# Performance work log

Measured on AMD Instinct MI355X. Metric: run time of the kernel, lower is better.

Reference implementation:

```python
import jax, jax.numpy as jnp
import numpy as np

# --- static config (matches init_kwargs) ---
C = 384        # channels
H = 8          # num_heads
HD = C // H    # head_dim = 48
K = 1024       # patch_size (window)
BASE = 100.0   # rope_freq
MAX_POS = 4096
GRID_SIZE = 0.02
LN_EPS = 1e-5


def _interleave8(x, y, z):
    """Morton-interleave the low 8 bits of x,y,z -> 24-bit code (int32)."""
    key = jnp.zeros_like(x)
    for i in range(8):
        m = 1 << i
        key = key | ((x & m) << (2 * i + 2)) | ((y & m) << (2 * i + 1)) | ((z & m) << (2 * i))
    return key


def _serialize_points(xyz):
    """xyz: (B,3,N) -> (order (B,N) int32, grid (B,N,3) int32). Z-order sort."""
    pts = jnp.transpose(xyz, (0, 2, 1))                       # (B,N,3)
    grid = ((pts - pts.min(axis=1, keepdims=True)) / GRID_SIZE).astype(jnp.int32)
    grid = jnp.clip(grid, 0, 65535)
    gx, gy, gz = grid[..., 0], grid[..., 1], grid[..., 2]
    lo = _interleave8(gx & 255, gy & 255, gz & 255)           # low 24 bits of Morton code
    hi = _interleave8((gx >> 8) & 255, (gy >> 8) & 255, (gz >> 8) & 255)  # high word
    # 48-bit Morton order == lexsort with hi as primary key, lo secondary
    order = jax.vmap(lambda l, h: jnp.lexsort((l, h)))(lo, hi)
    return order.astype(jnp.int32), grid


def _rope_tables(d):
    inv_freq = 1.0 / (BASE ** (jnp.arange(0, d, 2, dtype=jnp.float32) / d))
    t = jnp.arange(MAX_POS, dtype=jnp.float32)
    freqs = t[:, None] * inv_freq[None, :]                    # (MAX_POS, d/2)
    freqs = jnp.concatenate([freqs, freqs], axis=-1)          # (MAX_POS, d)
    return jnp.cos(freqs), jnp.sin(freqs)


def _rotate_half(x):
    h = x.shape[-1] // 2
    return jnp.concatenate([-x[..., h:], x[..., :h]], axis=-1)


def _point_rope(tok, pos):
    """tok: (B,H,N,D) with D%3==0; pos: (B,N,3) int grid coords."""
    D = tok.shape[-1]
    d = D // 3
    pos = jnp.clip(pos, 0, MAX_POS - 1)
    cos, sin = _rope_tables(d)
    outs = []
    for axis, ch in enumerate(jnp.split(tok, 3, axis=-1)):
        p = pos[:, :, axis]                                   # (B,N)
        c = cos[p][:, None]                                   # (B,1,N,d)
        s = sin[p][:, None]
        outs.append(ch * c + _rotate_half(ch) * s)
    return jnp.concatenate(outs, axis=-1)


def _layernorm(x, g, b):
    mu = x.mean(axis=-1, keepdims=True)
    var = ((x - mu) ** 2).mean(axis=-1, keepdims=True)
    return (x - mu) * jax.lax.rsqrt(var + LN_EPS) * g + b


def _forward(x, xyz, ln1_g, ln1_b, qkv_w, qkv_b, proj_w, proj_b,
             ln2_g, ln2_b, ffn_w1, ffn_b1, ffn_w2, ffn_b2):
    B, C_, N = x.shape
    order, grid = _serialize_points(xyz)
    x_sorted = jnp.take_along_axis(x, order[:, None, :], axis=2)          # (B,C,N)
    grid_sorted = jnp.take_along_axis(grid, order[:, :, None], axis=1)    # (B,N,3)
    x_t = jnp.transpose(x_sorted, (0, 2, 1))                              # (B,N,C)
    shortcut = x_t
    xn = _layernorm(x_t, ln1_g, ln1_b)
    pad = (K - N % K) % K
    if pad > 0:
        xn = jnp.pad(xn, ((0, 0), (0, pad), (0, 0)))
        grid_sorted = jnp.pad(grid_sorted, ((0, 0), (0, pad), (0, 0)))
    Np = xn.shape[1]
    nw = Np // K
    qkv = (xn @ qkv_w + qkv_b).reshape(B, Np, 3, H, HD)
    q = jnp.transpose(qkv[:, :, 0], (0, 2, 1, 3))                         # (B,H,Np,HD)
    k = jnp.transpose(qkv[:, :, 1], (0, 2, 1, 3))
    v = jnp.transpose(qkv[:, :, 2], (0, 2, 1, 3))
    q = _point_rope(q, grid_sorted)
    k = _point_rope(k, grid_sorted)
    qw = q.reshape(B, H, nw, K, HD)
    kw = k.reshape(B, H, nw, K, HD)
    vw = v.reshape(B, H, nw, K, HD)
    scale = 1.0 / np.sqrt(HD).astype(np.float32)
    scores = jnp.einsum('bhwqd,bhwkd->bhwqk', qw, kw) * scale             # (B,H,nw,K,K)
    attn = jax.nn.softmax(scores, axis=-1)
    out = jnp.einsum('bhwqk,bhwkd->bhwqd', attn, vw)                      # (B,H,nw,K,HD)
    out = jnp.transpose(out, (0, 2, 3, 1, 4)).reshape(B, Np, C)
    out = out[:, :N]
    out = out @ proj_w + proj_b
    x_t = shortcut + out
    x_t = x_t + (jax.nn.gelu(_layernorm(x_t, ln2_g, ln2_b) @ ffn_w1 + ffn_b1,
                             approximate=False) @ ffn_w2 + ffn_b2)
    x_out = jnp.transpose(x_t, (0, 2, 1))                                 # (B,C,N)
    inv_order = jnp.argsort(order, axis=1)
    x_out = jnp.take_along_axis(x_out, inv_order[:, None, :], axis=2)
    return x_out


def setup_inputs() -> dict:
    key = jax.random.key(0)
    ks = jax.random.split(key, 12)
    B, N = 1, 16384
    s = 0.02
    return {
        'x': jax.random.normal(ks[0], (B, C, N), dtype=jnp.float32),
        'xyz': jax.random.uniform(ks[1], (B, 3, N), dtype=jnp.float32),
        'ln1_g': jnp.ones((C,), jnp.float32),
        'ln1_b': jnp.zeros((C,), jnp.float32),
        'qkv_w': jax.random.normal(ks[2], (C, 3 * C), jnp.float32) * s,
        'qkv_b': jnp.zeros((3 * C,), jnp.float32),
        'proj_w': jax.random.normal(ks[3], (C, C), jnp.float32) * s,
        'proj_b': jnp.zeros((C,), jnp.float32),
        'ln2_g': jnp.ones((C,), jnp.float32),
        'ln2_b': jnp.zeros((C,), jnp.float32),
        'ffn_w1': jax.random.normal(ks[4], (C, 4 * C), jnp.float32) * s,
        'ffn_b1': jnp.zeros((4 * C,), jnp.float32),
        'ffn_w2': jax.random.normal(ks[5], (4 * C, C), jnp.float32) * s,
        'ffn_b2': jnp.zeros((C,), jnp.float32),
    }


def reference(x, xyz, ln1_g, ln1_b, qkv_w, qkv_b, proj_w, proj_b,
              ln2_g, ln2_b, ffn_w1, ffn_b1, ffn_w2, ffn_b2):
    return _forward(x, xyz, ln1_g, ln1_b, qkv_w, qkv_b, proj_w, proj_b,
                    ln2_g, ln2_b, ffn_w1, ffn_b1, ffn_w2, ffn_b2)
```

## Files before the change

### kernel.cpp

```cpp
#include <hip/hip_runtime.h>
#include <hip/hip_bf16.h>

typedef unsigned short u16;
typedef unsigned int u32;
typedef unsigned long long u64;
typedef __attribute__((ext_vector_type(8))) short s16x8;
typedef __attribute__((ext_vector_type(4))) short s16x4;
typedef __attribute__((ext_vector_type(8))) unsigned short u16x8;
typedef __attribute__((ext_vector_type(4))) unsigned short u16x4;
typedef __attribute__((ext_vector_type(4))) float fx4;
typedef __attribute__((ext_vector_type(4))) unsigned int ux4;
typedef __attribute__((ext_vector_type(2))) unsigned int ux2;

__device__ __forceinline__ float bf2f(u16 u){ u32 x=((u32)u)<<16; return __builtin_bit_cast(float,x); }
__device__ __forceinline__ u16 f2bf(float f){ u32 x=__builtin_bit_cast(u32,f); return (u16)((x + 0x7FFFu + ((x>>16)&1u))>>16); }
__device__ __forceinline__ u32 cvtpk(float lo, float hi){
  u32 r; asm("v_cvt_pk_bf16_f32 %0, %1, %2" : "=v"(r) : "v"(lo), "v"(hi)); return r;
}

__device__ __forceinline__ s16x8 ld_bf8(const u16* p){
  s16x4 lo = *(const s16x4*)p;
  s16x4 hi = *(const s16x4*)(p+4);
  s16x8 r;
  r[0]=lo[0]; r[1]=lo[1]; r[2]=lo[2]; r[3]=lo[3];
  r[4]=hi[0]; r[5]=hi[1]; r[6]=hi[2]; r[7]=hi[3];
  return r;
}

__device__ __forceinline__ void gload16(const void* g, void* l){
  __builtin_amdgcn_global_load_lds((__attribute__((address_space(1))) void*)g,
                                   (__attribute__((address_space(3))) void*)l, 16, 0, 0);
}

__device__ __forceinline__ u64 spread3(u32 v){
  u64 x = v & 0xFFFFull;
  x = (x | (x<<32)) & 0x001f00000000ffffull;
  x = (x | (x<<16)) & 0x001f0000ff0000ffull;
  x = (x | (x<<8))  & 0x100f00f00f00f00full;
  x = (x | (x<<4))  & 0x10c30c30c30c30c3ull;
  x = (x | (x<<2))  & 0x1249249249249249ull;
  return x;
}

__global__ __launch_bounds__(256) void min3_kernel(const float* __restrict__ xyz, u32* __restrict__ mins, int N)
{
  int i = blockIdx.x*256 + threadIdx.x;
  float v0 = xyz[i], v1 = xyz[N+i], v2 = xyz[2*N+i];
  #pragma unroll
  for (int s=1;s<64;s<<=1){
    v0 = fminf(v0, __shfl_xor(v0,s));
    v1 = fminf(v1, __shfl_xor(v1,s));
    v2 = fminf(v2, __shfl_xor(v2,s));
  }
  if ((threadIdx.x & 63) == 0){
    atomicMin(mins+0, __builtin_bit_cast(u32, v0));
    atomicMin(mins+1, __builtin_bit_cast(u32, v1));
    atomicMin(mins+2, __builtin_bit_cast(u32, v2));
  }
}

__global__ __launch_bounds__(256) void keys_grid_kernel(const float* __restrict__ xyz, const u32* __restrict__ mins,
        u64* __restrict__ keys, int* __restrict__ gridO, int N)
{
  int i = blockIdx.x*256 + threadIdx.x;
  float mx0 = __builtin_bit_cast(float, mins[0]);
  float mx1 = __builtin_bit_cast(float, mins[1]);
  float mx2 = __builtin_bit_cast(float, mins[2]);
  int gx=(int)((xyz[i]-mx0)/0.02f);     gx = gx<0?0:(gx>65535?65535:gx);
  int gy=(int)((xyz[N+i]-mx1)/0.02f);   gy = gy<0?0:(gy>65535?65535:gy);
  int gz=(int)((xyz[2*N+i]-mx2)/0.02f); gz = gz<0?0:(gz>65535?65535:gz);
  gridO[i*3+0]=gx; gridO[i*3+1]=gy; gridO[i*3+2]=gz;
  u64 mort = (spread3((u32)gx)<<2)|(spread3((u32)gy)<<1)|spread3((u32)gz);
  keys[i] = (mort<<14) | (u64)i;
}

__global__ __launch_bounds__(1024) void bsort_kernel(u64* __restrict__ keys)
{
  __shared__ u64 sk[2048];
  int t = threadIdx.x;
  u64* base = keys + (size_t)blockIdx.x*2048;
  sk[t] = base[t]; sk[t+1024] = base[t+1024];
  for (int size=2; size<=2048; size<<=1){
    for (int stride=size>>1; stride>0; stride>>=1){
      __syncthreads();
      int i = 2*t - (t & (stride-1));
      int j = i + stride;
      u64 a = sk[i], b = sk[j];
      bool up = ((i & size) == 0);
      if ((a > b) == up){ sk[i]=b; sk[j]=a; }
    }
  }
  __syncthreads();
  base[t] = sk[t]; base[t+1024] = sk[t+1024];
}

template<bool FINAL>
__global__ __launch_bounds__(256) void merge_kernel(const u64* __restrict__ src, u64* __restrict__ dst,
        int* __restrict__ order, int L, int N)
{
  int gt = blockIdx.x*256 + threadIdx.x;
  int d0 = gt*8;
  if (d0 >= N) return;
  int pair = d0 / (2*L);
  int base = pair*2*L;
  int ld = d0 - base;
  const u64* A = src + base;
  const u64* B = A + L;
  int lo = ld > L ? ld - L : 0;
  int hi = ld < L ? ld : L;
  while (lo < hi){
    int mid = (lo+hi)>>1;
    if (A[mid] <= B[ld-1-mid]) lo = mid+1; else hi = mid;
  }
  int i = lo, j = ld - lo;
  u64* out = dst + base + ld;
  int* oout = order + base + ld;
  u64 a = (i < L) ? A[i] : ~0ull;
  u64 b = (j < L) ? B[j] : ~0ull;
  #pragma unroll
  for (int e=0;e<8;e++){
    u64 v;
    if (a <= b){ v = a; i++; a = (i<L)?A[i]:~0ull; }
    else       { v = b; j++; b = (j<L)?B[j]:~0ull; }
    out[e] = v;
    if (FINAL) oout[e] = (int)(v & 16383ull);
  }
}

__global__ __launch_bounds__(256) void wtrans4_kernel(const float* __restrict__ qkv_w, const float* __restrict__ proj_w,
    const float* __restrict__ w1, const float* __restrict__ w2,
    u16* __restrict__ qkv_wT, u16* __restrict__ proj_wT, u16* __restrict__ w1T, u16* __restrict__ w2T)
{
  __shared__ float tl[32][33];
  int bid = blockIdx.x;
  const float* W; u16* Wt; int K, Nc, lb;
  if (bid < 432)      { W=qkv_w;  Wt=qkv_wT;  K=384;  Nc=1152; lb=bid; }
  else if (bid < 576) { W=proj_w; Wt=proj_wT; K=384;  Nc=384;  lb=bid-432; }
  else if (bid < 1152){ W=w1;     Wt=w1T;     K=384;  Nc=1536; lb=bid-576; }
  else                { W=w2;     Wt=w2T;     K=1536; Nc=384;  lb=bid-1152; }
  int nb = Nc/32;
  int n0 = (lb % nb)*32;
  int k0 = (lb / nb)*32;
  int t=threadIdx.x; int r=t>>5, c=t&31;
  #pragma unroll
  for (int p=0;p<4;p++) tl[p*8+r][c] = W[(size_t)(k0+p*8+r)*Nc + n0+c];
  __syncthreads();
  #pragma unroll
  for (int p=0;p<4;p++) Wt[(size_t)(n0+p*8+r)*K + k0+c] = f2bf(tl[c][p*8+r]);
}

template<bool BF16IN>
__global__ __launch_bounds__(256) void ln32_kernel(const void* __restrict__ xin, const float* __restrict__ g,
     const float* __restrict__ b, u16* __restrict__ xn, int N)
{
  extern __shared__ char dsm[];
  float* tile = (float*)dsm;
  int n0 = blockIdx.x*32;
  int t = threadIdx.x;
  int tok32 = t&31, cg2 = t>>5;
  #pragma unroll 8
  for (int p=0;p<48;p++){
    int cc = p*8 + cg2;
    float v;
    if (BF16IN) v = bf2f(((const u16*)xin)[(size_t)cc*N + n0 + tok32]);
    else        v = ((const float*)xin)[(size_t)cc*N + n0 + tok32];
    tile[tok32*388 + cc] = v;
  }
  __syncthreads();
  int tok = t>>3, part = t&7;
  const float* row = tile + tok*388 + part*48;
  float s=0.f;
  #pragma unroll
  for (int j=0;j<48;j++) s += row[j];
  s += __shfl_xor(s,1); s += __shfl_xor(s,2); s += __shfl_xor(s,4);
  float mu = s*(1.0f/384.0f);
  float vr=0.f;
  #pragma unroll
  for (int j=0;j<48;j++){ float d=row[j]-mu; vr += d*d; }
  vr += __shfl_xor(vr,1); vr += __shfl_xor(vr,2); vr += __shfl_xor(vr,4);
  float rs = rsqrtf(vr*(1.0f/384.0f) + 1e-5f);
  u16* dst = xn + (size_t)(n0+tok)*384 + part*48;
  #pragma unroll
  for (int q=0;q<6;q++){
    float v[8];
    #pragma unroll
    for (int j=0;j<8;j++){
      int c = part*48 + q*8 + j;
      v[j] = (row[q*8+j]-mu)*rs*g[c] + b[c];
    }
    ux4 o;
    o[0]=cvtpk(v[0],v[1]); o[1]=cvtpk(v[2],v[3]); o[2]=cvtpk(v[4],v[5]); o[3]=cvtpk(v[6],v[7]);
    *(ux4*)(dst + q*8) = o;
  }
}

__device__ __forceinline__ float gelu_f(float v){
  return 0.5f*v*(1.0f + erff(v*0.7071067811865475f));
}

template<int EPI>
__global__ __launch_bounds__(256) void gemm128_kernel(const u16* __restrict__ A, const u16* __restrict__ Bt,
    const float* __restrict__ bias, u16* __restrict__ outB, float* __restrict__ outF,
    const float* __restrict__ resF, const u16* __restrict__ resB, int M, int Nout, int K)
{
  __shared__ u16 Al[128*64];
  __shared__ u16 Bl[128*64];
  int nmt = M>>7;
  int m0 = (blockIdx.x % nmt)<<7;
  int n0 = (blockIdx.x / nmt)<<7;
  int t = threadIdx.x, lane=t&63, wv=t>>6, wr=wv>>1, wc=wv&1;
  int fr = lane&15, fg = lane>>4;
  fx4 acc[4][4];
  #pragma unroll
  for (int i=0;i<4;i++)
  #pragma unroll
  for (int j=0;j<4;j++) acc[i][j]=(fx4){0.f,0.f,0.f,0.f};
  int srow = wv*32 + (lane>>3);
  int swz  = ((lane&7) ^ ((lane>>3)&7)) * 8;
  const u16* ApL = A  + (size_t)(m0+srow)*K + swz;
  const u16* BpL = Bt + (size_t)(n0+srow)*K + swz;
  u16* AlW = Al + wv*2048 + lane*8;
  u16* BlW = Bl + wv*2048 + lane*8;
  const u16* a_base = Al + (wr*64+fr)*64;
  const u16* b_base = Bl + (wc*64+fr)*64;
  int swr = fr & 7;
  for (int k0=0;k0<K;k0+=64){
    #pragma unroll
    for (int i=0;i<4;i++){
      gload16(ApL + k0 + (size_t)i*8*K, AlW + i*512);
      gload16(BpL + k0 + (size_t)i*8*K, BlW + i*512);
    }
    __syncthreads();
    #pragma unroll
    for (int ks=0;ks<2;ks++){
      int soff = (((ks*4+fg) ^ swr) << 3);
      s16x8 a[4], b[4];
      #pragma unroll
      for (int mi=0;mi<4;mi++) a[mi] = *(const s16x8*)(a_base + mi*1024 + soff);
      #pragma unroll
      for (int ni=0;ni<4;ni++) b[ni] = *(const s16x8*)(b_base + ni*1024 + soff);
      #pragma unroll
      for (int mi=0;mi<4;mi++)
      #pragma unroll
      for (int ni=0;ni<4;ni++)
        acc[mi][ni] = __builtin_amdgcn_mfma_f32_16x16x32_bf16(a[mi], b[ni], acc[mi][ni], 0,0,0);
    }
    __syncthreads();
  }
  if (EPI==0 || EPI==1){
    #pragma unroll
    for (int mi=0;mi<4;mi++)
    #pragma unroll
    for (int ni=0;ni<4;ni++){
      int c = n0 + wc*64 + ni*16 + fr;
      float bi = bias[c];
      int mb = m0 + wr*64 + mi*16 + fg*4;
      #pragma unroll
      for (int j=0;j<4;j++){
        float vv = acc[mi][ni][j] + bi;
        if (EPI==1) vv = gelu_f(vv);
        outB[(size_t)(mb+j)*Nout + c] = f2bf(vv);
      }
    }
  } else if (EPI==2){
    #pragma unroll
    for (int mi=0;mi<4;mi++)
    #pragma unroll
    for (int ni=0;ni<4;ni++){
      int c = n0 + wc*64 + ni*16 + fr;
      float bi = bias[c];
      size_t idx = (size_t)c*M + m0 + wr*64 + mi*16 + fg*4;
      fx4 r4 = *(const fx4*)(resF + idx);
      ux2 p;
      p[0] = cvtpk(acc[mi][ni][0]+bi+r4[0], acc[mi][ni][1]+bi+r4[1]);
      p[1] = cvtpk(acc[mi][ni][2]+bi+r4[2], acc[mi][ni][3]+bi+r4[3]);
      *(ux2*)(outB + idx) = p;
    }
  } else {
    #pragma unroll
    for (int mi=0;mi<4;mi++)
    #pragma unroll
    for (int ni=0;ni<4;ni++){
      int c = n0 + wc*64 + ni*16 + fr;
      float bi = bias[c];
      size_t idx = (size_t)c*M + m0 + wr*64 + mi*16 + fg*4;
      ux2 rb = *(const ux2*)(resB + idx);
      fx4 o;
      o[0] = acc[mi][ni][0] + bi + bf2f((u16)rb[0]);
      o[1] = acc[mi][ni][1] + bi + bf2f((u16)(rb[0]>>16));
      o[2] = acc[mi][ni][2] + bi + bf2f((u16)rb[1]);
      o[3] = acc[mi][ni][3] + bi + bf2f((u16)(rb[1]>>16));
      *(fx4*)(outF + idx) = o;
    }
  }
}

#define LOG2_100_O8 0.8304820237218405f

__global__ __launch_bounds__(256) void rope_kernel(const u16* __restrict__ qkv, const int* __restrict__ order,
    const int* __restrict__ gridO, u16* __restrict__ Qp, u16* __restrict__ Kp, u16* __restrict__ Vp, int N)
{
  __shared__ float csm[64][24][2];
  __shared__ int origs[64];
  int i0 = blockIdx.x<<6;
  int t = threadIdx.x;
  if (t<64) origs[t] = order[i0+t];
  __syncthreads();
  for (int idx=t; idx<64*24; idx+=256){
    int tok = idx/24, slot = idx - tok*24;
    int a = slot>>3, fi = slot&7;
    int pos = gridO[(size_t)origs[tok]*3 + a];
    pos = pos<0?0:(pos>4095?4095:pos);
    float invf = __builtin_amdgcn_exp2f(-(float)fi * LOG2_100_O8);
    float ang = (float)pos * invf;
    csm[tok][slot][0] = __cosf(ang);
    csm[tok][slot][1] = __sinf(ang);
  }
  __syncthreads();
  int tok = t&63;
  int i = i0 + tok;
  const u16* src = qkv + (size_t)origs[tok]*1152;
  for (int h=t>>6; h<8; h+=4){
    size_t dst = ((size_t)h*N + i)*48;
    #pragma unroll
    for (int a=0;a<3;a++){
      u16x8 qa = *(const u16x8*)(src + h*48 + a*16);
      u16x8 qb = *(const u16x8*)(src + h*48 + a*16 + 8);
      u16x8 ka = *(const u16x8*)(src + 384 + h*48 + a*16);
      u16x8 kb = *(const u16x8*)(src + 384 + h*48 + a*16 + 8);
      float oqa[8], oqb[8], oka[8], okb[8];
      #pragma unroll
      for (int j=0;j<8;j++){
        float c0 = csm[tok][a*8+j][0], s0 = csm[tok][a*8+j][1];
        float ql = bf2f(qa[j]), qh = bf2f(qb[j]);
        float kl = bf2f(ka[j]), kh = bf2f(kb[j]);
        oqa[j] = ql*c0 - qh*s0;
        oqb[j] = qh*c0 + ql*s0;
        oka[j] = kl*c0 - kh*s0;
        okb[j] = kh*c0 + kl*s0;
      }
      ux4 OQa, OQb, OKa, OKb;
      #pragma unroll
      for (int p=0;p<4;p++){
        OQa[p]=cvtpk(oqa[2*p],oqa[2*p+1]);
        OQb[p]=cvtpk(oqb[2*p],oqb[2*p+1]);
        OKa[p]=cvtpk(oka[2*p],oka[2*p+1]);
        OKb[p]=cvtpk(okb[2*p],okb[2*p+1]);
      }
      *(ux4*)(Qp + dst + a*16) = OQa;
      *(ux4*)(Qp + dst + a*16 + 8) = OQb;
      *(ux4*)(Kp + dst + a*16) = OKa;
      *(ux4*)(Kp + dst + a*16 + 8) = OKb;
      u16x8 va = *(const u16x8*)(src + 768 + h*48 + a*16);
      u16x8 vb = *(const u16x8*)(src + 768 + h*48 + a*16 + 8);
      *(u16x8*)(Vp + dst + a*16) = va;
      *(u16x8*)(Vp + dst + a*16 + 8) = vb;
    }
  }
}

#define ATTN_SCALE 0.14433756729740643f
#define E2SCALE 0.2082354550504211f
#define DEFER_RAW 55.0f
#define KSTRIDE 68

__global__ __launch_bounds__(512) void attn7_kernel(const u16* __restrict__ Qp, const u16* __restrict__ Kp,
    const u16* __restrict__ Vp, const int* __restrict__ order, u16* __restrict__ attn, int N, int nw)
{
  __shared__ u16 Kl[2][64*KSTRIDE];
  __shared__ u16 Vl[2][48*KSTRIDE];
  __shared__ u16 Pl[8][32*KSTRIDE];
  int b = blockIdx.x;
  int hw = b & 127;
  int qc = b >> 7;
  int w = hw % nw, h = hw / nw;
  int t = threadIdx.x, lane = t&63, wv = t>>6;
  int fr = lane & 15, fg = lane >> 4;
  size_t base = ((size_t)h*N + (size_t)w*1024);
  int q0 = qc*256 + wv*32;
  bool kact = t < 384;
  int krow = t/6, kc = t - krow*6;
  const u16* ksrc = Kp + (base + krow)*48 + kc*8;
  int koff = krow*KSTRIDE + kc*8;
  int s2 = t - 128;
  bool vact = t >= 128;
  int vrow = s2/6, vc = s2 - vrow*6;
  const u16* vsrc = Vp + (base + vrow)*48 + vc*8;
  int vkey = vrow ^ (vc<<3);
  if (t < 256){
    ux2 z = {0,0};
    *(ux2*)&Kl[0][(t>>2)*KSTRIDE + 48 + (t&3)*4] = z;
    *(ux2*)&Kl[1][(t>>2)*KSTRIDE + 48 + (t&3)*4] = z;
  }
  s16x8 qf[2][2];
  s16x8 zf = {0,0,0,0,0,0,0,0};
  #pragma unroll
  for (int n=0;n<2;n++){
    const u16* qrow = Qp + (base + q0 + n*16 + fr)*48;
    qf[n][0] = ld_bf8(qrow + fg*8);
    qf[n][1] = (fg < 2) ? ld_bf8(qrow + 32 + fg*8) : zf;
  }
  s16x8 ones;
  #pragma unroll
  for (int j=0;j<8;j++) ones[j] = (short)0x3F80;

  float m0r = -3.4e38f, m1r = -3.4e38f;
  fx4 o00=(fx4){0.f,0.f,0.f,0.f}, o01=o00, o02=o00, o03=o00, o10=o00, o11=o00, o12=o00, o13=o00;
  u16* pl = Pl[wv];
  ux4 kreg = {0,0,0,0}, vreg = {0,0,0,0};
  if (kact) kreg = *(const ux4*)ksrc;
  if (vact) vreg = *(const ux4*)vsrc;
  if (kact){
    ux2 lo; lo[0]=kreg[0]; lo[1]=kreg[1];
    ux2 hi; hi[0]=kreg[2]; hi[1]=kreg[3];
    *(ux2*)(Kl[0]+koff) = lo; *(ux2*)(Kl[0]+koff+4) = hi;
  }
  if (vact){
    u16* vcp = Vl[0] + vkey;
    vcp[(vc*8+0)*KSTRIDE] = (u16)vreg[0];
    vcp[(vc*8+1)*KSTRIDE] = (u16)(vreg[0]>>16);
    vcp[(vc*8+2)*KSTRIDE] = (u16)vreg[1];
    vcp[(vc*8+3)*KSTRIDE] = (u16)(vreg[1]>>16);
    vcp[(vc*8+4)*KSTRIDE] = (u16)vreg[2];
    vcp[(vc*8+5)*KSTRIDE] = (u16)(vreg[2]>>16);
    vcp[(vc*8+6)*KSTRIDE] = (u16)vreg[3];
    vcp[(vc*8+7)*KSTRIDE] = (u16)(vreg[3]>>16);
  }
  __syncthreads();

  for (int c=0;c<16;c++){
    int cur = c & 1;
    const u16* kl = Kl[cur];
    const u16* vl = Vl[cur];
    if (c < 15){
      if (kact) kreg = *(const ux4*)(ksrc + (size_t)(c+1)*3072);
      if (vact) vreg = *(const ux4*)(vsrc + (size_t)(c+1)*3072);
    }
    fx4 s0[4], s1v[4];
    __builtin_amdgcn_s_setprio(1);
    #pragma unroll
    for (int m=0;m<4;m++){
      s0[m]=(fx4){0.f,0.f,0.f,0.f}; s1v[m]=s0[m];
      #pragma unroll
      for (int s=0;s<2;s++){
        s16x8 af = ld_bf8(kl + (m*16+fr)*KSTRIDE + s*32 + fg*8);
        s0[m]  = __builtin_amdgcn_mfma_f32_16x16x32_bf16(af, qf[0][s], s0[m],  0,0,0);
        s1v[m] = __builtin_amdgcn_mfma_f32_16x16x32_bf16(af, qf[1][s], s1v[m], 0,0,0);
      }
    }
    __builtin_amdgcn_s_setprio(0);
    float pm0 = -3.4e38f, pm1 = -3.4e38f;
    #pragma unroll
    for (int m=0;m<4;m++){
      float a0 = fmaxf(fmaxf(s0[m][0],s0[m][1]), fmaxf(s0[m][2],s0[m][3]));
      float a1 = fmaxf(fmaxf(s1v[m][0],s1v[m][1]), fmaxf(s1v[m][2],s1v[m][3]));
      pm0 = fmaxf(pm0, a0); pm1 = fmaxf(pm1, a1);
    }
    pm0 = fmaxf(pm0, __shfl_xor(pm0,16)); pm0 = fmaxf(pm0, __shfl_xor(pm0,32));
    pm1 = fmaxf(pm1, __shfl_xor(pm1,16)); pm1 = fmaxf(pm1, __shfl_xor(pm1,32));
    if (!__all((pm0 <= m0r + DEFER_RAW) & (pm1 <= m1r + DEFER_RAW))){
      float nm0 = fmaxf(m0r, pm0), nm1 = fmaxf(m1r, pm1);
      float f0 = __builtin_amdgcn_exp2f((m0r - nm0)*E2SCALE);
      float f1 = __builtin_amdgcn_exp2f((m1r - nm1)*E2SCALE);
      m0r = nm0; m1r = nm1;
      #pragma unroll
      for (int j=0;j<4;j++){
        float g0 = __shfl(f0, fg*4+j);
        float g1 = __shfl(f1, fg*4+j);
        o00[j]*=g0; o01[j]*=g0; o02[j]*=g0; o03[j]*=g0;
        o10[j]*=g1; o11[j]*=g1; o12[j]*=g1; o13[j]*=g1;
      }
    }
    #pragma unroll
    for (int m=0;m<4;m++){
      float e0[4], e1[4];
      #pragma unroll
      for (int j=0;j<4;j++){
        e0[j] = __builtin_amdgcn_exp2f((s0[m][j]-m0r)*E2SCALE);
        e1[j] = __builtin_amdgcn_exp2f((s1v[m][j]-m1r)*E2SCALE);
      }
      ux2 P0, P1;
      P0[0]=cvtpk(e0[0],e0[1]); P0[1]=cvtpk(e0[2],e0[3]);
      P1[0]=cvtpk(e1[0],e1[1]); P1[1]=cvtpk(e1[2],e1[3]);
      *(ux2*)&pl[(fr)*KSTRIDE + m*16 + fg*4]      = P0;
      *(ux2*)&pl[(16+fr)*KSTRIDE + m*16 + fg*4]   = P1;
    }
    __builtin_amdgcn_s_setprio(1);
    #pragma unroll
    for (int s=0;s<2;s++){
      int kb = s*32 + fg*8;
      s16x8 pa0 = ld_bf8(pl + fr*KSTRIDE + kb);
      s16x8 pa1 = ld_bf8(pl + (16+fr)*KSTRIDE + kb);
      s16x8 vb0 = ld_bf8(vl + (fr)*KSTRIDE    + (kb ^ ((fr)&56)));
      s16x8 vb1 = ld_bf8(vl + (16+fr)*KSTRIDE + (kb ^ ((16+fr)&56)));
      s16x8 vb2 = ld_bf8(vl + (32+fr)*KSTRIDE + (kb ^ ((32+fr)&56)));
      o00 = __builtin_amdgcn_mfma_f32_16x16x32_bf16(pa0, vb0, o00, 0,0,0);
      o01 = __builtin_amdgcn_mfma_f32_16x16x32_bf16(pa0, vb1, o01, 0,0,0);
      o02 = __builtin_amdgcn_mfma_f32_16x16x32_bf16(pa0, vb2, o02, 0,0,0);
      o03 = __builtin_amdgcn_mfma_f32_16x16x32_bf16(pa0, ones, o03, 0,0,0);
      o10 = __builtin_amdgcn_mfma_f32_16x16x32_bf16(pa1, vb0, o10, 0,0,0);
      o11 = __builtin_amdgcn_mfma_f32_16x16x32_bf16(pa1, vb1, o11, 0,0,0);
      o12 = __builtin_amdgcn_mfma_f32_16x16x32_bf16(pa1, vb2, o12, 0,0,0);
      o13 = __builtin_amdgcn_mfma_f32_16x16x32_bf16(pa1, ones, o13, 0,0,0);
    }
    __builtin_amdgcn_s_setprio(0);
    if (c < 15){
      u16* kln = Kl[cur^1];
      u16* vln = Vl[cur^1];
      if (kact){
        ux2 lo; lo[0]=kreg[0]; lo[1]=kreg[1];
        ux2 hi; hi[0]=kreg[2]; hi[1]=kreg[3];
        *(ux2*)(kln+koff) = lo; *(ux2*)(kln+koff+4) = hi;
      }
      if (vact){
        u16* vcp = vln + vkey;
        vcp[(vc*8+0)*KSTRIDE] = (u16)vreg[0];
        vcp[(vc*8+1)*KSTRIDE] = (u16)(vreg[0]>>16);
        vcp[(vc*8+2)*KSTRIDE] = (u16)vreg[1];
        vcp[(vc*8+3)*KSTRIDE] = (u16)(vreg[1]>>16);
        vcp[(vc*8+4)*KSTRIDE] = (u16)vreg[2];
        vcp[(vc*8+5)*KSTRIDE] = (u16)(vreg[2]>>16);
        vcp[(vc*8+6)*KSTRIDE] = (u16)vreg[3];
        vcp[(vc*8+7)*KSTRIDE] = (u16)(vreg[3]>>16);
      }
      __syncthreads();
    }
  }
  const int* ord = order + w*1024 + q0;
  #pragma unroll
  for (int j=0;j<4;j++){
    float inv0 = 1.0f / o03[j];
    float inv1 = 1.0f / o13[j];
    int orig0 = ord[fg*4+j];
    u16* dst0 = attn + (size_t)orig0*384 + h*48;
    dst0[fr]      = f2bf(o00[j]*inv0);
    dst0[16+fr]   = f2bf(o01[j]*inv0);
    dst0[32+fr]   = f2bf(o02[j]*inv0);
    int orig1 = ord[16 + fg*4+j];
    u16* dst1 = attn + (size_t)orig1*384 + h*48;
    dst1[fr]      = f2bf(o10[j]*inv1);
    dst1[16+fr]   = f2bf(o11[j]*inv1);
    dst1[32+fr]   = f2bf(o12[j]*inv1);
  }
}

extern "C" void kernel_launch(void* const* d_in, const int* in_sizes, int n_in,
                              void* d_out, int out_size, void* d_ws, size_t ws_size,
                              hipStream_t stream)
{
  (void)n_in; (void)out_size; (void)ws_size;
  const float* x     = (const float*)d_in[0];
  const float* xyz   = (const float*)d_in[1];
  const float* ln1_g = (const float*)d_in[2];
  const float* ln1_b = (const float*)d_in[3];
  const float* qkv_w = (const float*)d_in[4];
  const float* qkv_b = (const float*)d_in[5];
  const float* proj_w= (const float*)d_in[6];
  const float* proj_b= (const float*)d_in[7];
  const float* ln2_g = (const float*)d_in[8];
  const float* ln2_b = (const float*)d_in[9];
  const float* ffn_w1= (const float*)d_in[10];
  const float* ffn_b1= (const float*)d_in[11];
  const float* ffn_w2= (const float*)d_in[12];
  const float* ffn_b2= (const float*)d_in[13];
  int N = in_sizes[0]/384;
  int nw = N/1024;
  char* wsp = (char*)d_ws;
  size_t off = 0;
  auto alloc = [&](size_t bytes)->char*{ char* p = wsp + off; off = (off + bytes + 255) & ~(size_t)255; return p; };
  int*  order   = (int*)alloc((size_t)N*4);
  int*  gridO   = (int*)alloc((size_t)N*12);
  u32*  mins    = (u32*)alloc(256);
  u64*  keysA   = (u64*)alloc((size_t)N*8);
  u64*  keysB   = (u64*)alloc((size_t)N*8);
  u16*  qkv_wT  = (u16*)alloc((size_t)1152*384*2);
  u16*  proj_wT = (u16*)alloc((size_t)384*384*2);
  u16*  w1T     = (u16*)alloc((size_t)1536*384*2);
  u16*  w2T     = (u16*)alloc((size_t)384*1536*2);
  u16*  xn      = (u16*)alloc((size_t)N*384*2);
  u16*  Qp      = (u16*)alloc((size_t)N*48*8*2);
  u16*  Kp      = (u16*)alloc((size_t)N*48*8*2);
  u16*  Vp      = (u16*)alloc((size_t)N*48*8*2);
  u16*  qkvb    = (u16*)alloc((size_t)N*1152*2);
  u16*  y1b     = (u16*)alloc((size_t)N*384*2);
  u16*  attn    = xn;
  u16*  xn2     = qkvb;
  u16*  mid     = xn;
  float* outF = (float*)d_out;

  hipMemsetAsync(mins, 0xFF, 12, stream);
  min3_kernel<<<N/256, 256, 0, stream>>>(xyz, mins, N);
  keys_grid_kernel<<<N/256, 256, 0, stream>>>(xyz, mins, keysA, gridO, N);
  bsort_kernel<<<N/2048, 1024, 0, stream>>>(keysA);
  merge_kernel<false><<<N/2048, 256, 0, stream>>>(keysA, keysB, order, 2048, N);
  merge_kernel<false><<<N/2048, 256, 0, stream>>>(keysB, keysA, order, 4096, N);
  merge_kernel<true><<<N/2048, 256, 0, stream>>>(keysA, keysB, order, 8192, N);

  wtrans4_kernel<<<1728, 256, 0, stream>>>(qkv_w, proj_w, ffn_w1, ffn_w2, qkv_wT, proj_wT, w1T, w2T);
  ln32_kernel<false><<<N/32, 256, 32*388*4, stream>>>(x, ln1_g, ln1_b, xn, N);
  gemm128_kernel<0><<<(N/128)*(1152/128), 256, 0, stream>>>(xn, qkv_wT, qkv_b, qkvb, nullptr, nullptr, nullptr, N, 1152, 384);
  rope_kernel<<<N/64, 256, 0, stream>>>(qkvb, order, gridO, Qp, Kp, Vp, N);
  attn7_kernel<<<8*nw*4, 512, 0, stream>>>(Qp, Kp, Vp, order, attn, N, nw);
  gemm128_kernel<2><<<(N/128)*(384/128), 256, 0, stream>>>(attn, proj_wT, proj_b, y1b, nullptr, x, nullptr, N, 384, 384);
  ln32_kernel<true><<<N/32, 256, 32*388*4, stream>>>(y1b, ln2_g, ln2_b, xn2, N);
  gemm128_kernel<1><<<(N/128)*(1536/128), 256, 0, stream>>>(xn2, w1T, ffn_b1, mid, nullptr, nullptr, nullptr, N, 1536, 384);
  gemm128_kernel<3><<<(N/128)*(384/128), 256, 0, stream>>>(mid, w2T, ffn_b2, nullptr, outF, nullptr, y1b, N, 384, 1536);
}
```

Before: 291.7 us.

## Add 256x128-tile GEMM for QKV and FFN1, halve merge work per thread

Adds a 512-thread GEMM kernel with 256x128 output tiles, used for the QKV and FFN-up projections. Each weight tile loaded into LDS is now reused across twice as many rows, and the 8 waves per block give more latency hiding. The merge-sort kernels also produce 4 outputs per thread instead of 8 and launch twice as many blocks, adding parallelism to these small passes. The cost is more LDS per block (48KB) and fewer blocks in flight for the GEMMs.

```diff
diff --git a/kernel.cpp b/kernel.cpp
--- a/kernel.cpp
+++ b/kernel.cpp
@@ -99,7 +99,7 @@
         int* __restrict__ order, int L, int N)
 {
   int gt = blockIdx.x*256 + threadIdx.x;
-  int d0 = gt*8;
+  int d0 = gt*4;
   if (d0 >= N) return;
   int pair = d0 / (2*L);
   int base = pair*2*L;
@@ -118,7 +118,7 @@
   u64 a = (i < L) ? A[i] : ~0ull;
   u64 b = (j < L) ? B[j] : ~0ull;
   #pragma unroll
-  for (int e=0;e<8;e++){
+  for (int e=0;e<4;e++){
     u64 v;
     if (a <= b){ v = a; i++; a = (i<L)?A[i]:~0ull; }
     else       { v = b; j++; b = (j<L)?B[j]:~0ull; }
@@ -199,6 +199,70 @@
 }
 
 template<int EPI>
+__global__ __launch_bounds__(512) void gemm256_kernel(const u16* __restrict__ A, const u16* __restrict__ Bt,
+    const float* __restrict__ bias, u16* __restrict__ outB, int M, int Nout, int K)
+{
+  __shared__ u16 Al[256*64];
+  __shared__ u16 Bl[128*64];
+  int nmt = M>>8;
+  int m0 = (blockIdx.x % nmt)<<8;
+  int n0 = (blockIdx.x / nmt)<<7;
+  int t = threadIdx.x, lane=t&63, wv=t>>6, wr=wv>>1, wc=wv&1;
+  int fr = lane&15, fg = lane>>4;
+  fx4 acc[4][4];
+  #pragma unroll
+  for (int i=0;i<4;i++)
+  #pragma unroll
+  for (int j=0;j<4;j++) acc[i][j]=(fx4){0.f,0.f,0.f,0.f};
+  int srowA = wv*32 + (lane>>3);
+  int srowB = wv*16 + (lane>>3);
+  int swz  = ((lane&7) ^ ((lane>>3)&7)) * 8;
+  const u16* ApL = A  + (size_t)(m0+srowA)*K + swz;
+  const u16* BpL = Bt + (size_t)(n0+srowB)*K + swz;
+  u16* AlW = Al + wv*2048 + lane*8;
+  u16* BlW = Bl + wv*1024 + lane*8;
+  const u16* a_base = Al + (wr*64+fr)*64;
+  const u16* b_base = Bl + (wc*64+fr)*64;
+  int swr = fr & 7;
+  for (int k0=0;k0<K;k0+=64){
+    #pragma unroll
+    for (int i=0;i<4;i++) gload16(ApL + k0 + (size_t)i*8*K, AlW + i*512);
+    #pragma unroll
+    for (int i=0;i<2;i++) gload16(BpL + k0 + (size_t)i*8*K, BlW + i*512);
+    __syncthreads();
+    #pragma unroll
+    for (int ks=0;ks<2;ks++){
+      int soff = (((ks*4+fg) ^ swr) << 3);
+      s16x8 a[4], b[4];
+      #pragma unroll
+      for (int mi=0;mi<4;mi++) a[mi] = *(const s16x8*)(a_base + mi*1024 + soff);
+      #pragma unroll
+      for (int ni=0;ni<4;ni++) b[ni] = *(const s16x8*)(b_base + ni*1024 + soff);
+      #pragma unroll
+      for (int mi=0;mi<4;mi++)
+      #pragma unroll
+      for (int ni=0;ni<4;ni++)
+        acc[mi][ni] = __builtin_amdgcn_mfma_f32_16x16x32_bf16(a[mi], b[ni], acc[mi][ni], 0,0,0);
+    }
+    __syncthreads();
+  }
+  #pragma unroll
+  for (int mi=0;mi<4;mi++)
+  #pragma unroll
+  for (int ni=0;ni<4;ni++){
+    int c = n0 + wc*64 + ni*16 + fr;
+    float bi = bias[c];
+    int mb = m0 + wr*64 + mi*16 + fg*4;
+    #pragma unroll
+    for (int j=0;j<4;j++){
+      float vv = acc[mi][ni][j] + bi;
+      if (EPI==1) vv = gelu_f(vv);
+      outB[(size_t)(mb+j)*Nout + c] = f2bf(vv);
+    }
+  }
+}
+
+template<int EPI>
 __global__ __launch_bounds__(256) void gemm128_kernel(const u16* __restrict__ A, const u16* __restrict__ Bt,
     const float* __restrict__ bias, u16* __restrict__ outB, float* __restrict__ outF,
     const float* __restrict__ resF, const u16* __restrict__ resB, int M, int Nout, int K)
@@ -247,22 +311,7 @@
     }
     __syncthreads();
   }
-  if (EPI==0 || EPI==1){
-    #pragma unroll
-    for (int mi=0;mi<4;mi++)
-    #pragma unroll
-    for (int ni=0;ni<4;ni++){
-      int c = n0 + wc*64 + ni*16 + fr;
-      float bi = bias[c];
-      int mb = m0 + wr*64 + mi*16 + fg*4;
-      #pragma unroll
-      for (int j=0;j<4;j++){
-        float vv = acc[mi][ni][j] + bi;
-        if (EPI==1) vv = gelu_f(vv);
-        outB[(size_t)(mb+j)*Nout + c] = f2bf(vv);
-      }
-    }
-  } else if (EPI==2){
+  if (EPI==2){
     #pragma unroll
     for (int mi=0;mi<4;mi++)
     #pragma unroll
@@ -592,17 +641,17 @@
   min3_kernel<<<N/256, 256, 0, stream>>>(xyz, mins, N);
   keys_grid_kernel<<<N/256, 256, 0, stream>>>(xyz, mins, keysA, gridO, N);
   bsort_kernel<<<N/2048, 1024, 0, stream>>>(keysA);
-  merge_kernel<false><<<N/2048, 256, 0, stream>>>(keysA, keysB, order, 2048, N);
-  merge_kernel<false><<<N/2048, 256, 0, stream>>>(keysB, keysA, order, 4096, N);
-  merge_kernel<true><<<N/2048, 256, 0, stream>>>(keysA, keysB, order, 8192, N);
+  merge_kernel<false><<<N/1024, 256, 0, stream>>>(keysA, keysB, order, 2048, N);
+  merge_kernel<false><<<N/1024, 256, 0, stream>>>(keysB, keysA, order, 4096, N);
+  merge_kernel<true><<<N/1024, 256, 0, stream>>>(keysA, keysB, order, 8192, N);
 
   wtrans4_kernel<<<1728, 256, 0, stream>>>(qkv_w, proj_w, ffn_w1, ffn_w2, qkv_wT, proj_wT, w1T, w2T);
   ln32_kernel<false><<<N/32, 256, 32*388*4, stream>>>(x, ln1_g, ln1_b, xn, N);
-  gemm128_kernel<0><<<(N/128)*(1152/128), 256, 0, stream>>>(xn, qkv_wT, qkv_b, qkvb, nullptr, nullptr, nullptr, N, 1152, 384);
+  gemm256_kernel<0><<<(N/256)*(1152/128), 512, 0, stream>>>(xn, qkv_wT, qkv_b, qkvb, N, 1152, 384);
   rope_kernel<<<N/64, 256, 0, stream>>>(qkvb, order, gridO, Qp, Kp, Vp, N);
   attn7_kernel<<<8*nw*4, 512, 0, stream>>>(Qp, Kp, Vp, order, attn, N, nw);
   gemm128_kernel<2><<<(N/128)*(384/128), 256, 0, stream>>>(attn, proj_wT, proj_b, y1b, nullptr, x, nullptr, N, 384, 384);
   ln32_kernel<true><<<N/32, 256, 32*388*4, stream>>>(y1b, ln2_g, ln2_b, xn2, N);
-  gemm128_kernel<1><<<(N/128)*(1536/128), 256, 0, stream>>>(xn2, w1T, ffn_b1, mid, nullptr, nullptr, nullptr, N, 1536, 384);
+  gemm256_kernel<1><<<(N/256)*(1536/128), 512, 0, stream>>>(xn2, w1T, ffn_b1, mid, N, 1536, 384);
   gemm128_kernel<3><<<(N/128)*(384/128), 256, 0, stream>>>(mid, w2T, ffn_b2, nullptr, outF, nullptr, y1b, N, 384, 1536);
 }
```

Result: faster. 282.8 us (-3.1%).
